# Optimization experiments

Measured on AMD Instinct MI355X. Metric: run time of the kernel, lower is better.

The kernel has to match this reference:

```python
import jax, jax.numpy as jnp
import numpy as np

N_NODES = 50000
N_EDGES = 800000
NUM_GRAPHS = 512
D_IN = 64
D_H = 64
BN_EPS = 1e-5


def setup_inputs() -> dict:
    key = jax.random.key(0)
    ks = jax.random.split(key, 12)
    x = jax.random.normal(ks[0], (N_NODES, D_IN), dtype=jnp.float32)
    edge_index = jax.random.randint(ks[1], (2, N_EDGES), 0, N_NODES, dtype=jnp.int64)
    batch = jnp.sort(jax.random.randint(ks[2], (N_NODES,), 0, NUM_GRAPHS, dtype=jnp.int64))
    s1 = 1.0 / np.sqrt(D_IN)
    s2 = 1.0 / np.sqrt(D_H)
    s3 = 1.0 / np.sqrt(2 * D_H)
    W1 = jax.random.uniform(ks[3], (D_IN, D_H), jnp.float32, -s1, s1)
    b1 = jax.random.uniform(ks[4], (D_H,), jnp.float32, -s1, s1)
    gamma = jnp.ones((D_H,), jnp.float32)
    beta = jnp.zeros((D_H,), jnp.float32)
    W2 = jax.random.uniform(ks[5], (D_H, D_H), jnp.float32, -s2, s2)
    b2 = jax.random.uniform(ks[6], (D_H,), jnp.float32, -s2, s2)
    Wl1 = jax.random.uniform(ks[7], (2 * D_H, 2 * D_H), jnp.float32, -s3, s3)
    bl1 = jax.random.uniform(ks[8], (2 * D_H,), jnp.float32, -s3, s3)
    Wl2 = jax.random.uniform(ks[9], (2 * D_H, 1), jnp.float32, -s3, s3)
    bl2 = jax.random.uniform(ks[10], (1,), jnp.float32, -s3, s3)
    return {"x": x, "edge_index": edge_index, "batch": batch,
            "W1": W1, "b1": b1, "gamma": gamma, "beta": beta,
            "W2": W2, "b2": b2, "Wl1": Wl1, "bl1": bl1, "Wl2": Wl2, "bl2": bl2}


def reference(x, edge_index, batch, W1, b1, gamma, beta, W2, b2, Wl1, bl1, Wl2, bl2):
    src, dst = edge_index[0], edge_index[1]
    # GINConv with eps=0: (1+eps)*x_i + sum_{j->i} x_j
    agg = x + jax.ops.segment_sum(x[src], dst, num_segments=N_NODES)
    # MLP: Linear -> BatchNorm1d (training stats, biased var) -> ReLU -> Linear -> ReLU
    h = agg @ W1 + b1
    mean = jnp.mean(h, axis=0)
    var = jnp.var(h, axis=0)
    h = (h - mean) * jax.lax.rsqrt(var + BN_EPS) * gamma + beta
    h = jax.nn.relu(h)
    h = jax.nn.relu(h @ W2 + b2)
    # global add/max pooling per graph
    h_add = jax.ops.segment_sum(h, batch, num_segments=NUM_GRAPHS)
    h_max = jax.ops.segment_max(h, batch, num_segments=NUM_GRAPHS)
    g = jnp.concatenate((h_add, h_max), axis=1)  # [G, 2*D_H]
    g = jax.nn.relu(g @ Wl1 + bl1)
    logits = g @ Wl2 + bl2  # [G, 1]
    return (jax.nn.sigmoid(logits), logits)
```

## Files before the change

kernel.cpp:

```cpp
#include <hip/hip_runtime.h>
#include <hip/hip_bf16.h>

#define N_NODES 50000
#define N_EDGES 800000
#define NUM_GRAPHS 512
#define D 64
#define BN_EPS 1e-5f

#define BUK_SHIFT 7
#define BUK_SIZE 128
#define NBUK ((N_NODES + BUK_SIZE - 1) / BUK_SIZE)
#define CHUNK_A 4096
#define NBLK_A ((N_EDGES + CHUNK_A - 1) / CHUNK_A)

__global__ __launch_bounds__(512) void k_zero(int* __restrict__ bcnt,
                                              float* __restrict__ bnacc ,
                                              int* __restrict__ offs) {
    int t = threadIdx.x;
    for (int j = t; j < NBUK; j += 512) bcnt[j] = 0;
    if (t < 128) bnacc[t] = 0.0f;
    if (t == 0) offs[N_NODES] = N_EDGES;
}

__global__ __launch_bounds__(256) void k_bhist(const int* __restrict__ ei,
                                               int* __restrict__ bcnt) {
    __shared__ int h[NBUK];
    int t = threadIdx.x;
    for (int j = t; j < NBUK; j += 256) h[j] = 0;
    __syncthreads();
    int e0 = blockIdx.x * CHUNK_A;
#pragma unroll
    for (int i = 0; i < CHUNK_A / 256; i++) {
        int e = e0 + i * 256 + t;
        if (e < N_EDGES) atomicAdd(&h[ei[N_EDGES + e] >> BUK_SHIFT], 1);
    }
    __syncthreads();
    for (int j = t; j < NBUK; j += 256)
        if (h[j]) atomicAdd(&bcnt[j], h[j]);
}

__global__ __launch_bounds__(512) void k_bscan(const int* __restrict__ bcnt,
                                               int* __restrict__ boffs,
                                               int* __restrict__ gcur) {
    __shared__ int sm[512];
    int t = threadIdx.x;
    int v = (t < NBUK) ? bcnt[t] : 0;
    sm[t] = v;
    __syncthreads();
    for (int off = 1; off < 512; off <<= 1) {
        int a = sm[t];
        int u = (t >= off) ? sm[t - off] : 0;
        __syncthreads();
        sm[t] = a + u;
        __syncthreads();
    }
    if (t < NBUK) { int ex = sm[t] - v; boffs[t] = ex; gcur[t] = ex; }
    if (t == 0) boffs[NBUK] = N_EDGES;
}

__global__ __launch_bounds__(256) void k_binA(const int* __restrict__ ei,
                                              int* __restrict__ gcur,
                                              unsigned* __restrict__ pairs) {
    __shared__ int cnt[NBUK];
    __shared__ int base[NBUK];
    int t = threadIdx.x;
    for (int j = t; j < NBUK; j += 256) cnt[j] = 0;
    __syncthreads();
    int e0 = blockIdx.x * CHUNK_A;
    unsigned pd[CHUNK_A / 256];
    int loc[CHUNK_A / 256];
#pragma unroll
    for (int i = 0; i < CHUNK_A / 256; i++) {
        int e = e0 + i * 256 + t;
        pd[i] = 0xFFFFFFFFu;
        if (e < N_EDGES) {
            unsigned s = (unsigned)ei[e];
            unsigned d = (unsigned)ei[N_EDGES + e];
            pd[i] = (d << 16) | s;
            loc[i] = atomicAdd(&cnt[d >> BUK_SHIFT], 1);
        }
    }
    __syncthreads();
    for (int j = t; j < NBUK; j += 256)
        base[j] = cnt[j] ? atomicAdd(&gcur[j], cnt[j]) : 0;
    __syncthreads();
#pragma unroll
    for (int i = 0; i < CHUNK_A / 256; i++) {
        if (pd[i] != 0xFFFFFFFFu) {
            unsigned d = pd[i] >> 16;
            pairs[base[d >> BUK_SHIFT] + loc[i]] =
                ((d & (BUK_SIZE - 1)) << 16) | (pd[i] & 0xFFFFu);
        }
    }
}

__global__ __launch_bounds__(256) void k_sort(const unsigned* __restrict__ pairs,
                                              const int* __restrict__ boffs,
                                              int* __restrict__ offs,
                                              int* __restrict__ esrc) {
    __shared__ int cnt[BUK_SIZE];
    __shared__ int sm[BUK_SIZE];
    __shared__ int cur[BUK_SIZE];
    int b = blockIdx.x, t = threadIdx.x;
    int n0 = b << BUK_SHIFT;
    int nrows = min(BUK_SIZE, N_NODES - n0);
    int e0 = boffs[b], e1 = boffs[b + 1];
    int m = e1 - e0;
    if (t < BUK_SIZE) cnt[t] = 0;
    __syncthreads();
    for (int j = t; j < m; j += 256)
        atomicAdd(&cnt[pairs[e0 + j] >> 16], 1);
    __syncthreads();
    if (t < BUK_SIZE) sm[t] = cnt[t];
    __syncthreads();
    for (int off = 1; off < BUK_SIZE; off <<= 1) {
        int v = 0, u = 0;
        if (t < BUK_SIZE) { v = sm[t]; u = (t >= off) ? sm[t - off] : 0; }
        __syncthreads();
        if (t < BUK_SIZE) sm[t] = v + u;
        __syncthreads();
    }
    if (t < BUK_SIZE) {
        int ex = sm[t] - cnt[t];
        cur[t] = ex;
        if (t < nrows) offs[n0 + t] = e0 + ex;
    }
    __syncthreads();
    for (int j = t; j < m; j += 256) {
        unsigned p = pairs[e0 + j];
        int pos = atomicAdd(&cur[p >> 16], 1);
        esrc[e0 + pos] = (int)(p & 0xFFFFu);
    }
}

__global__ __launch_bounds__(256) void k_gather(const float* __restrict__ x,
                                                const int* __restrict__ offs,
                                                const int* __restrict__ esrc,
                                                float* __restrict__ agg) {
    int wid = (blockIdx.x * 256 + threadIdx.x) >> 6;
    int c = threadIdx.x & 63;
    if (wid >= N_NODES) return;
    int base = offs[wid];
    int end = offs[wid + 1];
    float acc = x[(size_t)wid * D + c];
    int i = base;
    for (; i + 3 < end; i += 4) {
        int s0 = esrc[i], s1 = esrc[i + 1], s2 = esrc[i + 2], s3 = esrc[i + 3];
        float v0 = x[(size_t)s0 * D + c];
        float v1 = x[(size_t)s1 * D + c];
        float v2 = x[(size_t)s2 * D + c];
        float v3 = x[(size_t)s3 * D + c];
        acc += v0; acc += v1; acc += v2; acc += v3;
    }
    for (; i < end; i++) acc += x[(size_t)esrc[i] * D + c];
    agg[(size_t)wid * D + c] = acc;
}

__global__ __launch_bounds__(256) void k_gemm1(const float* __restrict__ agg,
                                               const float* __restrict__ W1,
                                               const float* __restrict__ b1,
                                               float* __restrict__ hT) {
    int r = blockIdx.x * 256 + threadIdx.x;
    if (r >= N_NODES) return;
    float row[D];
#pragma unroll
    for (int k4 = 0; k4 < D / 4; k4++) {
        float4 v = *(const float4*)(agg + (size_t)r * D + k4 * 4);
        row[k4 * 4 + 0] = v.x; row[k4 * 4 + 1] = v.y;
        row[k4 * 4 + 2] = v.z; row[k4 * 4 + 3] = v.w;
    }
    for (int c4 = 0; c4 < D / 4; c4++) {
        float acc[4];
#pragma unroll
        for (int j = 0; j < 4; j++) acc[j] = b1[c4 * 4 + j];
#pragma unroll
        for (int k = 0; k < D; k++) {
#pragma unroll
            for (int j = 0; j < 4; j++)
                acc[j] += row[k] * W1[k * D + c4 * 4 + j];
        }
#pragma unroll
        for (int j = 0; j < 4; j++)
            hT[(size_t)(c4 * 4 + j) * N_NODES + r] = acc[j];
    }
}

__global__ __launch_bounds__(256) void k_bnstats(const float* __restrict__ hT,
                                                 float* __restrict__ bnsum,
                                                 float* __restrict__ bnsq) {
    __shared__ float ls[256], lq[256];
    int c = blockIdx.y;
    const float* p = hT + (size_t)c * N_NODES;
    float s = 0.f, q = 0.f;
    for (int i = blockIdx.x * 256 + threadIdx.x; i < N_NODES; i += 256 * gridDim.x) {
        float v = p[i];
        s += v; q += v * v;
    }
    int t = threadIdx.x;
    ls[t] = s; lq[t] = q;
    __syncthreads();
    for (int off = 128; off; off >>= 1) {
        if (t < off) { ls[t] += ls[t + off]; lq[t] += lq[t + off]; }
        __syncthreads();
    }
    if (t == 0) { atomicAdd(&bnsum[c], ls[0]); atomicAdd(&bnsq[c], lq[0]); }
}

__global__ void k_bnfinal(const float* __restrict__ bnsum, const float* __restrict__ bnsq,
                          const float* __restrict__ gamma, const float* __restrict__ beta,
                          float* __restrict__ bnscale, float* __restrict__ bnshift) {
    int c = threadIdx.x;
    float mean = bnsum[c] * (1.0f / N_NODES);
    float var  = bnsq[c] * (1.0f / N_NODES) - mean * mean;
    float rstd = rsqrtf(var + BN_EPS);
    float sc = gamma[c] * rstd;
    bnscale[c] = sc;
    bnshift[c] = beta[c] - mean * sc;
}

__global__ __launch_bounds__(256) void k_gemm2(const float* __restrict__ hT,
                                               const float* __restrict__ bnscale,
                                               const float* __restrict__ bnshift,
                                               const float* __restrict__ W2,
                                               const float* __restrict__ b2,
                                               float* __restrict__ h2T) {
    int r = blockIdx.x * 256 + threadIdx.x;
    if (r >= N_NODES) return;
    float row[D];
#pragma unroll
    for (int k = 0; k < D; k++) {
        float v = hT[(size_t)k * N_NODES + r];
        row[k] = fmaxf(v * bnscale[k] + bnshift[k], 0.0f);
    }
    for (int c4 = 0; c4 < D / 4; c4++) {
        float acc[4];
#pragma unroll
        for (int j = 0; j < 4; j++) acc[j] = b2[c4 * 4 + j];
#pragma unroll
        for (int k = 0; k < D; k++) {
#pragma unroll
            for (int j = 0; j < 4; j++)
                acc[j] += row[k] * W2[k * D + c4 * 4 + j];
        }
#pragma unroll
        for (int j = 0; j < 4; j++)
            h2T[(size_t)(c4 * 4 + j) * N_NODES + r] = fmaxf(acc[j], 0.0f);
    }
}

__device__ __forceinline__ int lower_bound(const int* __restrict__ b, int v) {
    int lo = 0, hi = N_NODES;
    while (lo < hi) {
        int m = (lo + hi) >> 1;
        if (b[m] < v) lo = m + 1; else hi = m;
    }
    return lo;
}

__global__ __launch_bounds__(64) void k_pool(const float* __restrict__ h2T,
                                             const int* __restrict__ batch,
                                             float* __restrict__ g) {
    int gi = blockIdx.x;
    int c = threadIdx.x;
    int s0 = lower_bound(batch, gi);
    int s1 = lower_bound(batch, gi + 1);
    const float* p = h2T + (size_t)c * N_NODES;
    float sm = 0.0f, mx = 0.0f;
    for (int n = s0; n < s1; n++) {
        float v = p[n];
        sm += v;
        mx = fmaxf(mx, v);
    }
    g[gi * 128 + c] = sm;
    g[gi * 128 + 64 + c] = mx;
}

__global__ __launch_bounds__(128) void k_head(const float* __restrict__ g,
                                              const float* __restrict__ Wl1,
                                              const float* __restrict__ bl1,
                                              const float* __restrict__ Wl2,
                                              const float* __restrict__ bl2,
                                              float* __restrict__ out) {
    __shared__ float gv[128];
    __shared__ float red[2];
    int gi = blockIdx.x;
    int t = threadIdx.x;
    gv[t] = g[gi * 128 + t];
    __syncthreads();
    float acc = bl1[t];
#pragma unroll
    for (int k = 0; k < 128; k++)
        acc += gv[k] * Wl1[k * 128 + t];
    acc = fmaxf(acc, 0.0f);
    float part = acc * Wl2[t];
    for (int off = 32; off; off >>= 1) part += __shfl_down(part, off);
    if ((t & 63) == 0) red[t >> 6] = part;
    __syncthreads();
    if (t == 0) {
        float logit = red[0] + red[1] + bl2[0];
        out[gi] = 1.0f / (1.0f + expf(-logit));
        out[NUM_GRAPHS + gi] = logit;
    }
}

extern "C" void kernel_launch(void* const* d_in, const int* in_sizes, int n_in,
                              void* d_out, int out_size, void* d_ws, size_t ws_size,
                              hipStream_t stream) {
    const float* x     = (const float*)d_in[0];
    const int*   ei    = (const int*)d_in[1];
    const int*   batch = (const int*)d_in[2];
    const float* W1    = (const float*)d_in[3];
    const float* b1    = (const float*)d_in[4];
    const float* gamma = (const float*)d_in[5];
    const float* beta  = (const float*)d_in[6];
    const float* W2    = (const float*)d_in[7];
    const float* b2    = (const float*)d_in[8];
    const float* Wl1   = (const float*)d_in[9];
    const float* bl1   = (const float*)d_in[10];
    const float* Wl2   = (const float*)d_in[11];
    const float* bl2   = (const float*)d_in[12];
    float* out = (float*)d_out;

    float* ws = (float*)d_ws;
    float* agg    = ws;
    float* hT     = agg + (size_t)N_NODES * D;
    float* gbuf   = hT + (size_t)N_NODES * D;
    float* bnsum  = gbuf + NUM_GRAPHS * 128;
    float* bnsq   = bnsum + 64;
    float* bnscale= bnsq + 64;
    float* bnshift= bnscale + 64;
    int*   bcnt   = (int*)(bnshift + 64);
    int*   boffs  = bcnt + NBUK;
    int*   gcur   = boffs + NBUK + 1;
    int*   offs   = gcur + NBUK;
    int*   esrc   = offs + N_NODES + 1;
    unsigned* pairs = (unsigned*)hT;
    float* h2T    = agg;

    k_zero <<<1, 512, 0, stream>>>(bcnt, bnsum, offs);
    k_bhist<<<NBLK_A, 256, 0, stream>>>(ei, bcnt);
    k_bscan<<<1, 512, 0, stream>>>(bcnt, boffs, gcur);
    k_binA <<<NBLK_A, 256, 0, stream>>>(ei, gcur, pairs);
    k_sort <<<NBUK, 256, 0, stream>>>(pairs, boffs, offs, esrc);
    k_gather<<<(N_NODES * 64 + 255) / 256, 256, 0, stream>>>(x, offs, esrc, agg);
    k_gemm1<<<(N_NODES + 255) / 256, 256, 0, stream>>>(agg, W1, b1, hT);
    k_bnstats<<<dim3(8, 64), 256, 0, stream>>>(hT, bnsum, bnsq);
    k_bnfinal<<<1, 64, 0, stream>>>(bnsum, bnsq, gamma, beta, bnscale, bnshift);
    k_gemm2<<<(N_NODES + 255) / 256, 256, 0, stream>>>(hT, bnscale, bnshift, W2, b2, h2T);
    k_pool <<<NUM_GRAPHS, 64, 0, stream>>>(h2T, batch, gbuf);
    k_head <<<NUM_GRAPHS, 128, 0, stream>>>(gbuf, Wl1, bl1, Wl2, bl2, out);
}
```

Measured before the change: 253.8 us.

## Switch node features to row-major and tile GEMMs through shared memory

Intermediate node features h and h2 move from a transposed column-major layout to row-major. Both dense GEMMs now stage a 64-row tile in LDS and have each thread compute 16 output columns with vectorized float4 stores. BN statistics use per-block partial sums reduced in a final kernel, which removes the atomics and the zeroing of the accumulators. Pooling splits each graph's nodes across 4 waves. The aim is coalesced loads and stores and less redundant per-thread work, at the cost of an extra partial-sum buffer in the workspace and possible bank pressure from the padded LDS tile.

```diff
diff --git a/kernel.cpp b/kernel.cpp
--- a/kernel.cpp
+++ b/kernel.cpp
@@ -12,13 +12,13 @@
 #define NBUK ((N_NODES + BUK_SIZE - 1) / BUK_SIZE)
 #define CHUNK_A 4096
 #define NBLK_A ((N_EDGES + CHUNK_A - 1) / CHUNK_A)
+#define GBLK ((N_NODES + 63) / 64)
+#define SBLK 256
 
 __global__ __launch_bounds__(512) void k_zero(int* __restrict__ bcnt,
-                                              float* __restrict__ bnacc ,
                                               int* __restrict__ offs) {
     int t = threadIdx.x;
     for (int j = t; j < NBUK; j += 512) bcnt[j] = 0;
-    if (t < 128) bnacc[t] = 0.0f;
     if (t == 0) offs[N_NODES] = N_EDGES;
 }
 
@@ -159,92 +159,130 @@
 __global__ __launch_bounds__(256) void k_gemm1(const float* __restrict__ agg,
                                                const float* __restrict__ W1,
                                                const float* __restrict__ b1,
-                                               float* __restrict__ hT) {
-    int r = blockIdx.x * 256 + threadIdx.x;
-    if (r >= N_NODES) return;
-    float row[D];
-#pragma unroll
-    for (int k4 = 0; k4 < D / 4; k4++) {
-        float4 v = *(const float4*)(agg + (size_t)r * D + k4 * 4);
-        row[k4 * 4 + 0] = v.x; row[k4 * 4 + 1] = v.y;
-        row[k4 * 4 + 2] = v.z; row[k4 * 4 + 3] = v.w;
-    }
-    for (int c4 = 0; c4 < D / 4; c4++) {
-        float acc[4];
-#pragma unroll
-        for (int j = 0; j < 4; j++) acc[j] = b1[c4 * 4 + j];
-#pragma unroll
-        for (int k = 0; k < D; k++) {
-#pragma unroll
-            for (int j = 0; j < 4; j++)
-                acc[j] += row[k] * W1[k * D + c4 * 4 + j];
+                                               float* __restrict__ h) {
+    __shared__ float xs[64][65];
+    int blk = blockIdx.x, t = threadIdx.x;
+    int r0 = blk * 64;
+    const float4* a4 = (const float4*)(agg + (size_t)r0 * D);
+    for (int i = t; i < 1024; i += 256) {
+        float4 v = a4[i];
+        int row = i >> 4, q = (i & 15) * 4;
+        xs[row][q] = v.x; xs[row][q + 1] = v.y;
+        xs[row][q + 2] = v.z; xs[row][q + 3] = v.w;
+    }
+    __syncthreads();
+    int lane = t & 63, chunk = t >> 6;
+    int r = r0 + lane;
+    int c0 = chunk * 16;
+    float acc[16];
+#pragma unroll
+    for (int j = 0; j < 16; j++) acc[j] = b1[c0 + j];
+#pragma unroll 4
+    for (int k = 0; k < D; k++) {
+        float v = xs[lane][k];
+#pragma unroll
+        for (int j = 0; j < 16; j++)
+            acc[j] += v * W1[k * D + c0 + j];
+    }
+    if (r < N_NODES) {
+        float* hp = h + (size_t)r * D + c0;
+#pragma unroll
+        for (int j4 = 0; j4 < 4; j4++) {
+            float4 o;
+            o.x = acc[j4 * 4]; o.y = acc[j4 * 4 + 1];
+            o.z = acc[j4 * 4 + 2]; o.w = acc[j4 * 4 + 3];
+            *(float4*)(hp + j4 * 4) = o;
         }
-#pragma unroll
-        for (int j = 0; j < 4; j++)
-            hT[(size_t)(c4 * 4 + j) * N_NODES + r] = acc[j];
-    }
-}
-
-__global__ __launch_bounds__(256) void k_bnstats(const float* __restrict__ hT,
-                                                 float* __restrict__ bnsum,
-                                                 float* __restrict__ bnsq) {
-    __shared__ float ls[256], lq[256];
-    int c = blockIdx.y;
-    const float* p = hT + (size_t)c * N_NODES;
+    }
+}
+
+__global__ __launch_bounds__(256) void k_bnstats(const float* __restrict__ h,
+                                                 float* __restrict__ partial) {
+    int t = threadIdx.x, w = t >> 6, c = t & 63;
     float s = 0.f, q = 0.f;
-    for (int i = blockIdx.x * 256 + threadIdx.x; i < N_NODES; i += 256 * gridDim.x) {
-        float v = p[i];
+    for (int n = blockIdx.x * 4 + w; n < N_NODES; n += SBLK * 4) {
+        float v = h[(size_t)n * D + c];
         s += v; q += v * v;
     }
-    int t = threadIdx.x;
-    ls[t] = s; lq[t] = q;
-    __syncthreads();
-    for (int off = 128; off; off >>= 1) {
-        if (t < off) { ls[t] += ls[t + off]; lq[t] += lq[t + off]; }
-        __syncthreads();
-    }
-    if (t == 0) { atomicAdd(&bnsum[c], ls[0]); atomicAdd(&bnsq[c], lq[0]); }
-}
-
-__global__ void k_bnfinal(const float* __restrict__ bnsum, const float* __restrict__ bnsq,
-                          const float* __restrict__ gamma, const float* __restrict__ beta,
-                          float* __restrict__ bnscale, float* __restrict__ bnshift) {
-    int c = threadIdx.x;
-    float mean = bnsum[c] * (1.0f / N_NODES);
-    float var  = bnsq[c] * (1.0f / N_NODES) - mean * mean;
-    float rstd = rsqrtf(var + BN_EPS);
-    float sc = gamma[c] * rstd;
-    bnscale[c] = sc;
-    bnshift[c] = beta[c] - mean * sc;
-}
-
-__global__ __launch_bounds__(256) void k_gemm2(const float* __restrict__ hT,
+    __shared__ float shS[4][64], shQ[4][64];
+    shS[w][c] = s; shQ[w][c] = q;
+    __syncthreads();
+    if (w == 0) {
+        float ts = shS[0][c] + shS[1][c] + shS[2][c] + shS[3][c];
+        float tq = shQ[0][c] + shQ[1][c] + shQ[2][c] + shQ[3][c];
+        partial[blockIdx.x * 128 + c] = ts;
+        partial[blockIdx.x * 128 + 64 + c] = tq;
+    }
+}
+
+__global__ __launch_bounds__(512) void k_bnfinal(const float* __restrict__ partial,
+                                                 const float* __restrict__ gamma,
+                                                 const float* __restrict__ beta,
+                                                 float* __restrict__ bnscale,
+                                                 float* __restrict__ bnshift) {
+    __shared__ float sh[4][128];
+    __shared__ float tot[128];
+    int t = threadIdx.x, c = t & 127, sl = t >> 7;
+    float s = 0.f;
+    for (int b = sl; b < SBLK; b += 4) s += partial[b * 128 + c];
+    sh[sl][c] = s;
+    __syncthreads();
+    if (t < 128) tot[t] = sh[0][t] + sh[1][t] + sh[2][t] + sh[3][t];
+    __syncthreads();
+    if (t < 64) {
+        float mean = tot[t] * (1.0f / N_NODES);
+        float var  = tot[64 + t] * (1.0f / N_NODES) - mean * mean;
+        float rstd = rsqrtf(var + BN_EPS);
+        float sc = gamma[t] * rstd;
+        bnscale[t] = sc;
+        bnshift[t] = beta[t] - mean * sc;
+    }
+}
+
+__global__ __launch_bounds__(256) void k_gemm2(const float* __restrict__ h,
                                                const float* __restrict__ bnscale,
                                                const float* __restrict__ bnshift,
                                                const float* __restrict__ W2,
                                                const float* __restrict__ b2,
-                                               float* __restrict__ h2T) {
-    int r = blockIdx.x * 256 + threadIdx.x;
-    if (r >= N_NODES) return;
-    float row[D];
-#pragma unroll
+                                               float* __restrict__ h2) {
+    __shared__ float xs[64][65];
+    __shared__ float bs[64], bb[64];
+    int blk = blockIdx.x, t = threadIdx.x;
+    if (t < 64) { bs[t] = bnscale[t]; bb[t] = bnshift[t]; }
+    __syncthreads();
+    int r0 = blk * 64;
+    const float4* a4 = (const float4*)(h + (size_t)r0 * D);
+    for (int i = t; i < 1024; i += 256) {
+        float4 v = a4[i];
+        int row = i >> 4, q = (i & 15) * 4;
+        xs[row][q]     = fmaxf(v.x * bs[q]     + bb[q],     0.0f);
+        xs[row][q + 1] = fmaxf(v.y * bs[q + 1] + bb[q + 1], 0.0f);
+        xs[row][q + 2] = fmaxf(v.z * bs[q + 2] + bb[q + 2], 0.0f);
+        xs[row][q + 3] = fmaxf(v.w * bs[q + 3] + bb[q + 3], 0.0f);
+    }
+    __syncthreads();
+    int lane = t & 63, chunk = t >> 6;
+    int r = r0 + lane;
+    int c0 = chunk * 16;
+    float acc[16];
+#pragma unroll
+    for (int j = 0; j < 16; j++) acc[j] = b2[c0 + j];
+#pragma unroll 4
     for (int k = 0; k < D; k++) {
-        float v = hT[(size_t)k * N_NODES + r];
-        row[k] = fmaxf(v * bnscale[k] + bnshift[k], 0.0f);
-    }
-    for (int c4 = 0; c4 < D / 4; c4++) {
-        float acc[4];
-#pragma unroll
-        for (int j = 0; j < 4; j++) acc[j] = b2[c4 * 4 + j];
-#pragma unroll
-        for (int k = 0; k < D; k++) {
-#pragma unroll
-            for (int j = 0; j < 4; j++)
-                acc[j] += row[k] * W2[k * D + c4 * 4 + j];
+        float v = xs[lane][k];
+#pragma unroll
+        for (int j = 0; j < 16; j++)
+            acc[j] += v * W2[k * D + c0 + j];
+    }
+    if (r < N_NODES) {
+        float* hp = h2 + (size_t)r * D + c0;
+#pragma unroll
+        for (int j4 = 0; j4 < 4; j4++) {
+            float4 o;
+            o.x = fmaxf(acc[j4 * 4], 0.0f);     o.y = fmaxf(acc[j4 * 4 + 1], 0.0f);
+            o.z = fmaxf(acc[j4 * 4 + 2], 0.0f); o.w = fmaxf(acc[j4 * 4 + 3], 0.0f);
+            *(float4*)(hp + j4 * 4) = o;
         }
-#pragma unroll
-        for (int j = 0; j < 4; j++)
-            h2T[(size_t)(c4 * 4 + j) * N_NODES + r] = fmaxf(acc[j], 0.0f);
     }
 }
 
@@ -257,22 +295,26 @@
     return lo;
 }
 
-__global__ __launch_bounds__(64) void k_pool(const float* __restrict__ h2T,
-                                             const int* __restrict__ batch,
-                                             float* __restrict__ g) {
-    int gi = blockIdx.x;
-    int c = threadIdx.x;
+__global__ __launch_bounds__(256) void k_pool(const float* __restrict__ h2,
+                                              const int* __restrict__ batch,
+                                              float* __restrict__ g) {
+    int gi = blockIdx.x, t = threadIdx.x, w = t >> 6, c = t & 63;
     int s0 = lower_bound(batch, gi);
     int s1 = lower_bound(batch, gi + 1);
-    const float* p = h2T + (size_t)c * N_NODES;
-    float sm = 0.0f, mx = 0.0f;
-    for (int n = s0; n < s1; n++) {
-        float v = p[n];
-        sm += v;
-        mx = fmaxf(mx, v);
-    }
-    g[gi * 128 + c] = sm;
-    g[gi * 128 + 64 + c] = mx;
+    float sm = 0.f, mx = 0.f;
+    for (int n = s0 + w; n < s1; n += 4) {
+        float v = h2[(size_t)n * D + c];
+        sm += v; mx = fmaxf(mx, v);
+    }
+    __shared__ float shS[4][64], shM[4][64];
+    shS[w][c] = sm; shM[w][c] = mx;
+    __syncthreads();
+    if (w == 0) {
+        float ts = shS[0][c] + shS[1][c] + shS[2][c] + shS[3][c];
+        float tm = fmaxf(fmaxf(shM[0][c], shM[1][c]), fmaxf(shM[2][c], shM[3][c]));
+        g[gi * 128 + c] = ts;
+        g[gi * 128 + 64 + c] = tm;
+    }
 }
 
 __global__ __launch_bounds__(128) void k_head(const float* __restrict__ g,
@@ -323,30 +365,29 @@
 
     float* ws = (float*)d_ws;
     float* agg    = ws;
-    float* hT     = agg + (size_t)N_NODES * D;
-    float* gbuf   = hT + (size_t)N_NODES * D;
-    float* bnsum  = gbuf + NUM_GRAPHS * 128;
-    float* bnsq   = bnsum + 64;
-    float* bnscale= bnsq + 64;
+    float* h      = agg + (size_t)N_NODES * D;
+    float* gbuf   = h + (size_t)N_NODES * D;
+    float* bnscale= gbuf + NUM_GRAPHS * 128;
     float* bnshift= bnscale + 64;
     int*   bcnt   = (int*)(bnshift + 64);
     int*   boffs  = bcnt + NBUK;
     int*   gcur   = boffs + NBUK + 1;
     int*   offs   = gcur + NBUK;
     int*   esrc   = offs + N_NODES + 1;
-    unsigned* pairs = (unsigned*)hT;
-    float* h2T    = agg;
-
-    k_zero <<<1, 512, 0, stream>>>(bcnt, bnsum, offs);
-    k_bhist<<<NBLK_A, 256, 0, stream>>>(ei, bcnt);
-    k_bscan<<<1, 512, 0, stream>>>(bcnt, boffs, gcur);
-    k_binA <<<NBLK_A, 256, 0, stream>>>(ei, gcur, pairs);
-    k_sort <<<NBUK, 256, 0, stream>>>(pairs, boffs, offs, esrc);
-    k_gather<<<(N_NODES * 64 + 255) / 256, 256, 0, stream>>>(x, offs, esrc, agg);
-    k_gemm1<<<(N_NODES + 255) / 256, 256, 0, stream>>>(agg, W1, b1, hT);
-    k_bnstats<<<dim3(8, 64), 256, 0, stream>>>(hT, bnsum, bnsq);
-    k_bnfinal<<<1, 64, 0, stream>>>(bnsum, bnsq, gamma, beta, bnscale, bnshift);
-    k_gemm2<<<(N_NODES + 255) / 256, 256, 0, stream>>>(hT, bnscale, bnshift, W2, b2, h2T);
-    k_pool <<<NUM_GRAPHS, 64, 0, stream>>>(h2T, batch, gbuf);
-    k_head <<<NUM_GRAPHS, 128, 0, stream>>>(gbuf, Wl1, bl1, Wl2, bl2, out);
-}
+    float* partial= (float*)(esrc + N_EDGES);
+    unsigned* pairs = (unsigned*)h;
+    float* h2     = agg;
+
+    k_zero   <<<1, 512, 0, stream>>>(bcnt, offs);
+    k_bhist  <<<NBLK_A, 256, 0, stream>>>(ei, bcnt);
+    k_bscan  <<<1, 512, 0, stream>>>(bcnt, boffs, gcur);
+    k_binA   <<<NBLK_A, 256, 0, stream>>>(ei, gcur, pairs);
+    k_sort   <<<NBUK, 256, 0, stream>>>(pairs, boffs, offs, esrc);
+    k_gather <<<(N_NODES * 64 + 255) / 256, 256, 0, stream>>>(x, offs, esrc, agg);
+    k_gemm1  <<<GBLK, 256, 0, stream>>>(agg, W1, b1, h);
+    k_bnstats<<<SBLK, 256, 0, stream>>>(h, partial);
+    k_bnfinal<<<1, 512, 0, stream>>>(partial, gamma, beta, bnscale, bnshift);
+    k_gemm2  <<<GBLK, 256, 0, stream>>>(h, bnscale, bnshift, W2, b2, h2);
+    k_pool   <<<NUM_GRAPHS, 256, 0, stream>>>(h2, batch, gbuf);
+    k_head   <<<NUM_GRAPHS, 128, 0, stream>>>(gbuf, Wl1, bl1, Wl2, bl2, out);
+}
```

Measured after the change: 277.9 us. +9.5%, slower.
